# Kernel optimization log

Measured on AMD Instinct MI355X. Metric: run time of the kernel, lower is better.

Reference implementation:

```python
import jax, jax.numpy as jnp
import numpy as np

B, N, M, D = 8, 4096, 256, 1024
H, HD, ROT = 16, 64, 32  # heads, head_dim, rotary dim (partial_rotary_factor=0.5)
GRID_H = GRID_W = 64     # sqrt(N)
BASE = 10000


def rope_tables_2d(h, w, rot_dim, base=BASE, dtype=jnp.float32):
    # 2D rope: half the rotary channels encode height, half encode width.
    n_freq = rot_dim // 4
    inv = 1.0 / (base ** (jnp.arange(n_freq, dtype=jnp.float32) / n_freq))
    fh = jnp.arange(h, dtype=jnp.float32)[:, None] * inv          # [h, nf]
    fw = jnp.arange(w, dtype=jnp.float32)[:, None] * inv          # [w, nf]
    fh_g = jnp.broadcast_to(fh[:, None, :], (h, w, n_freq))
    fw_g = jnp.broadcast_to(fw[None, :, :], (h, w, n_freq))
    freqs = jnp.concatenate([fh_g, fw_g], -1).reshape(h * w, rot_dim // 2)
    emb = jnp.concatenate([freqs, freqs], -1)                     # [h*w, rot_dim]
    return jnp.cos(emb).astype(dtype), jnp.sin(emb).astype(dtype)


def rotate_half(x):
    x1, x2 = jnp.split(x, 2, axis=-1)
    return jnp.concatenate([-x2, x1], axis=-1)


def layernorm(x, w, b, eps=1e-5):
    mu = x.mean(-1, keepdims=True)
    var = ((x - mu) ** 2).mean(-1, keepdims=True)
    return (x - mu) * jax.lax.rsqrt(var + eps) * w + b


def setup_inputs() -> dict:
    key = jax.random.key(0)
    ks = jax.random.split(key, 5)
    inner = H * HD
    return {
        "x": jax.random.normal(ks[0], (B, N, D), jnp.float32),
        "latents": jax.random.normal(ks[1], (B, M, D), jnp.float32),
        "ln_x_w": jnp.ones((D,), jnp.float32),
        "ln_x_b": jnp.zeros((D,), jnp.float32),
        "ln_l_w": jnp.ones((D,), jnp.float32),
        "ln_l_b": jnp.zeros((D,), jnp.float32),
        "Wq": jax.random.normal(ks[2], (D, inner), jnp.float32) * (D ** -0.5),
        "Wkv": jax.random.normal(ks[3], (D, 2 * inner), jnp.float32) * (D ** -0.5),
        "Wo": jax.random.normal(ks[4], (inner, D), jnp.float32) * (inner ** -0.5),
    }


def reference(x, latents, ln_x_w, ln_x_b, ln_l_w, ln_l_b, Wq, Wkv, Wo):
    scale = HD ** -0.5
    xn = layernorm(x, ln_x_w, ln_x_b)
    ln = layernorm(latents, ln_l_w, ln_l_b)

    q = ln @ Wq                                   # [B, M, H*HD]
    kv_x = xn @ Wkv                               # [B, N, 2*H*HD]
    kv_l = ln @ Wkv                               # [B, M, 2*H*HD]
    k_x, v_x = jnp.split(kv_x, 2, axis=-1)
    k_l, v_l = jnp.split(kv_l, 2, axis=-1)

    def to_bhnd(t, L):
        return t.reshape(t.shape[0], L, H, HD).transpose(0, 2, 1, 3)

    q = to_bhnd(q, M)                             # [B, H, M, HD]
    k_x = to_bhnd(k_x, N)                         # [B, H, N, HD]
    v_x = to_bhnd(v_x, N)
    k_l = to_bhnd(k_l, M)
    v_l = to_bhnd(v_l, M)

    # partial 2D RoPE on input keys only (first ROT channels)
    cos, sin = rope_tables_2d(GRID_H, GRID_W, ROT)  # [N, ROT]
    k_rope, k_pass = k_x[..., :ROT], k_x[..., ROT:]
    k_rope = k_rope * cos + rotate_half(k_rope) * sin
    k_x = jnp.concatenate([k_rope, k_pass], axis=-1)

    k = jnp.concatenate([k_x, k_l], axis=2)       # [B, H, N+M, HD]
    v = jnp.concatenate([v_x, v_l], axis=2)

    sim = jnp.einsum('bhid,bhjd->bhij', q * scale, k)   # [B, H, M, N+M]
    attn = jax.nn.softmax(sim, axis=-1)
    out = jnp.einsum('bhij,bhjd->bhid', attn, v)        # [B, H, M, HD]
    out = out.transpose(0, 2, 1, 3).reshape(out.shape[0], M, H * HD)
    return out @ Wo                                      # [B, M, D]
```

## Files before the change

kernel.cpp:

```cpp
#include <hip/hip_runtime.h>
#include <hip/hip_bf16.h>

#define Bb 8
#define Nn 4096
#define Mm 256
#define Dd 1024
#define Hh 16
#define HDd 64
#define Ss 4352
#define INNERd 1024
#define SPLIT 8

typedef __attribute__((ext_vector_type(4))) float f32x4;
typedef __attribute__((ext_vector_type(8))) short short8;
typedef __attribute__((ext_vector_type(4))) int int4v;

__device__ __forceinline__ float bf2f(short u) {
  union { unsigned int i; float f; } c;
  c.i = ((unsigned int)(unsigned short)u) << 16;
  return c.f;
}
__device__ __forceinline__ short f2bf(float f) {
  union { float f; unsigned int i; } c; c.f = f;
  unsigned int x = c.i;
  x += 0x7fff + ((x >> 16) & 1);
  return (short)(x >> 16);
}
__device__ __forceinline__ void gload16(const short* g, short* l) {
  __builtin_amdgcn_global_load_lds(
      (const __attribute__((address_space(1))) void*)g,
      (__attribute__((address_space(3))) void*)l, 16, 0, 0);
}

__global__ __launch_bounds__(256) void prep_kernel(
    const float* __restrict__ x, const float* __restrict__ lat,
    const float* __restrict__ lnxw, const float* __restrict__ lnxb,
    const float* __restrict__ lnlw, const float* __restrict__ lnlb,
    const float* __restrict__ Wq, const float* __restrict__ Wkv,
    const float* __restrict__ Wo,
    short* __restrict__ xn, short* __restrict__ lnr,
    short* __restrict__ Wqkvt, short* __restrict__ Wot) {
  __shared__ float shbuf[32 * 33];
  int b = blockIdx.x, t = threadIdx.x;
  if (b < 34816) {
    const float *src, *w, *bv; short* dst; int row;
    if (b < 32768) { src = x;   w = lnxw; bv = lnxb; dst = xn;  row = b; }
    else           { src = lat; w = lnlw; bv = lnlb; dst = lnr; row = b - 32768; }
    const float4* x4 = (const float4*)(src + (size_t)row * Dd);
    float4 v = x4[t];
    float s  = v.x + v.y + v.z + v.w;
    float ss = v.x*v.x + v.y*v.y + v.z*v.z + v.w*v.w;
#pragma unroll
    for (int o = 1; o < 64; o <<= 1) {
      s  += __shfl_xor(s,  o, 64);
      ss += __shfl_xor(ss, o, 64);
    }
    int wv = t >> 6;
    if ((t & 63) == 0) { shbuf[wv] = s; shbuf[4 + wv] = ss; }
    __syncthreads();
    float tot  = shbuf[0] + shbuf[1] + shbuf[2] + shbuf[3];
    float tot2 = shbuf[4] + shbuf[5] + shbuf[6] + shbuf[7];
    float mean = tot * (1.0f / Dd);
    float var  = tot2 * (1.0f / Dd) - mean * mean;
    float inv  = rsqrtf(var + 1e-5f);
    float4 wv4 = ((const float4*)w)[t];
    float4 bv4 = ((const float4*)bv)[t];
    short4 o4;
    o4.x = f2bf((v.x - mean) * inv * wv4.x + bv4.x);
    o4.y = f2bf((v.y - mean) * inv * wv4.y + bv4.y);
    o4.z = f2bf((v.z - mean) * inv * wv4.z + bv4.z);
    o4.w = f2bf((v.w - mean) * inv * wv4.w + bv4.w);
    *(short4*)(dst + (size_t)row * Dd + t * 4) = o4;
  } else {
    int tb = b - 34816;
    const float* src; short* dst; int Ncol, bx, by;
    if (tb < 1024)      { src = Wq;  dst = Wqkvt; Ncol = 1024; bx = tb & 31; by = tb >> 5; }
    else if (tb < 3072) { int u = tb - 1024; src = Wkv; dst = Wqkvt + (size_t)1024 * 1024; Ncol = 2048; bx = u & 63; by = u >> 6; }
    else                { int u = tb - 3072; src = Wo;  dst = Wot; Ncol = 1024; bx = u & 31; by = u >> 5; }
    int tx = t & 31, ty = t >> 5;
#pragma unroll
    for (int i = 0; i < 32; i += 8)
      shbuf[(ty + i) * 33 + tx] = src[(size_t)(by * 32 + ty + i) * Ncol + bx * 32 + tx];
    __syncthreads();
#pragma unroll
    for (int i = 0; i < 32; i += 8)
      dst[(size_t)(bx * 32 + ty + i) * 1024 + by * 32 + tx] = f2bf(shbuf[tx * 33 + ty + i]);
  }
}

__global__ __launch_bounds__(256, 4) void gemm_fused_kernel(
    const short* __restrict__ xn, const short* __restrict__ lnr,
    const short* __restrict__ Wkvt, const short* __restrict__ Wqkvt,
    short* __restrict__ qdst, short* __restrict__ kdst, short* __restrict__ vdst) {
  __shared__ __align__(16) short Asm[128 * 64];
  __shared__ __align__(16) short Bsm[128 * 64];
  __shared__ float ctab[1024];
  int t = threadIdx.x;
  int wave = t >> 6, lane = t & 63;
  int wm = (wave >> 1) * 64, wn = (wave & 1) * 64;
  int lr = lane & 15, lg = lane >> 4;
  bool big = (int)blockIdx.x < 4096;
  const short* A  = big ? xn  : lnr;
  const short* Bt = big ? Wkvt : Wqkvt;
  int bid = big ? blockIdx.x : blockIdx.x - 4096;
  int nwg = big ? 4096 : 384;
  int ncp = big ? 16 : 24;
  int cpx = nwg >> 3;
  int swz = (bid & 7) * cpx + (bid >> 3);
  int colp = swz % ncp, rowp = swz / ncp;
  int brow = rowp * 128, bcol = colp * 128;
  if (big) {
#pragma unroll
    for (int i = t; i < 512; i += 256) {
      int pos = i >> 3, f = i & 7;
      float ang = (float)pos * exp2f(-1.6609640474436813f * (float)f);
      ctab[i] = cosf(ang);
      ctab[512 + i] = sinf(ang);
    }
  }
  f32x4 acc[4][4] = {};
  for (int kt = 0; kt < 1024; kt += 64) {
    __syncthreads();
#pragma unroll
    for (int u = 0; u < 4; u++) {
      int cid = t + u * 256;
      int r = cid >> 3, c = cid & 7;
      int cl = c ^ (r & 7);
      gload16(A + (size_t)(brow + r) * 1024 + kt + cl * 8, Asm + cid * 8);
      gload16(Bt + (size_t)(bcol + r) * 1024 + kt + cl * 8, Bsm + cid * 8);
    }
    __syncthreads();
#pragma unroll
    for (int ks = 0; ks < 2; ks++) {
      short8 a[4], b[4];
#pragma unroll
      for (int i = 0; i < 4; i++) {
        int ra = wm + i * 16 + lr;
        a[i] = *(const short8*)(Asm + ra * 64 + (((ks * 4 + lg) ^ (ra & 7)) * 8));
        int rb = wn + i * 16 + lr;
        b[i] = *(const short8*)(Bsm + rb * 64 + (((ks * 4 + lg) ^ (rb & 7)) * 8));
      }
#pragma unroll
      for (int mi = 0; mi < 4; mi++)
#pragma unroll
        for (int ni = 0; ni < 4; ni++)
          acc[mi][ni] = __builtin_amdgcn_mfma_f32_16x16x32_bf16(a[mi], b[ni], acc[mi][ni], 0, 0, 0);
    }
  }
  int cbase = bcol + wn;
  if (big) {
    bool kreg = cbase < 1024;
    short* dstp = kreg ? kdst : vdst;
    int h = (cbase & 1023) >> 6;
#pragma unroll
    for (int mi = 0; mi < 4; mi++)
#pragma unroll
      for (int rr = 0; rr < 4; rr++) {
        int row = brow + wm + mi * 16 + lg * 4 + rr;
        int bb = row >> 12, n = row & 4095;
        float v[4];
#pragma unroll
        for (int ni = 0; ni < 4; ni++) v[ni] = acc[mi][ni][rr];
        if (kreg) {
          int pos = (lr & 8) ? (n & 63) : (n >> 6);
          float cs = ctab[pos * 8 + (lr & 7)];
          float sn = ctab[512 + pos * 8 + (lr & 7)];
          float v0 = v[0], v1 = v[1];
          v[0] = v0 * cs - v1 * sn;
          v[1] = v1 * cs + v0 * sn;
        }
        size_t rb = (((size_t)(bb * Hh + h)) * Ss + n) * HDd;
#pragma unroll
        for (int ni = 0; ni < 4; ni++)
          dstp[rb + ni * 16 + lr] = f2bf(v[ni]);
      }
  } else {
#pragma unroll
    for (int mi = 0; mi < 4; mi++)
#pragma unroll
      for (int rr = 0; rr < 4; rr++) {
        int row = brow + wm + mi * 16 + lg * 4 + rr;
        int bb = row >> 8, m = row & 255;
        float v[4];
#pragma unroll
        for (int ni = 0; ni < 4; ni++) v[ni] = acc[mi][ni][rr];
        if (cbase < 1024) {
          int h = cbase >> 6;
          size_t rb = (((size_t)(bb * Hh + h)) * Mm + m) * HDd;
#pragma unroll
          for (int ni = 0; ni < 4; ni++)
            qdst[rb + ni * 16 + lr] = f2bf(v[ni] * 0.18033688f);
        } else if (cbase < 2048) {
          int h = (cbase - 1024) >> 6;
          size_t rb = (((size_t)(bb * Hh + h)) * Ss + (Nn + m)) * HDd;
#pragma unroll
          for (int ni = 0; ni < 4; ni++)
            kdst[rb + ni * 16 + lr] = f2bf(v[ni]);
        } else {
          int h = (cbase - 2048) >> 6;
          size_t rb = (((size_t)(bb * Hh + h)) * Ss + (Nn + m)) * HDd;
#pragma unroll
          for (int ni = 0; ni < 4; ni++)
            vdst[rb + ni * 16 + lr] = f2bf(v[ni]);
        }
      }
  }
}

__global__ __launch_bounds__(256, 4) void gemm_out_kernel(
    const short* __restrict__ A, const short* __restrict__ Bt,
    float* __restrict__ C, int ncp) {
  __shared__ __align__(16) short Asm[128 * 64];
  __shared__ __align__(16) short Bsm[128 * 64];
  int t = threadIdx.x;
  int wave = t >> 6, lane = t & 63;
  int wm = (wave >> 1) * 64, wn = (wave & 1) * 64;
  int lr = lane & 15, lg = lane >> 4;
  int nwg = gridDim.x;
  int cpx = nwg >> 3;
  int swz = (blockIdx.x & 7) * cpx + (blockIdx.x >> 3);
  int colp = swz % ncp, rowp = swz / ncp;
  int brow = rowp * 128, bcol = colp * 128;
  f32x4 acc[4][4] = {};
  for (int kt = 0; kt < 1024; kt += 64) {
    __syncthreads();
#pragma unroll
    for (int u = 0; u < 4; u++) {
      int cid = t + u * 256;
      int r = cid >> 3, c = cid & 7;
      int cl = c ^ (r & 7);
      gload16(A + (size_t)(brow + r) * 1024 + kt + cl * 8, Asm + cid * 8);
      gload16(Bt + (size_t)(bcol + r) * 1024 + kt + cl * 8, Bsm + cid * 8);
    }
    __syncthreads();
#pragma unroll
    for (int ks = 0; ks < 2; ks++) {
      short8 a[4], b[4];
#pragma unroll
      for (int i = 0; i < 4; i++) {
        int ra = wm + i * 16 + lr;
        a[i] = *(const short8*)(Asm + ra * 64 + (((ks * 4 + lg) ^ (ra & 7)) * 8));
        int rb = wn + i * 16 + lr;
        b[i] = *(const short8*)(Bsm + rb * 64 + (((ks * 4 + lg) ^ (rb & 7)) * 8));
      }
#pragma unroll
      for (int mi = 0; mi < 4; mi++)
#pragma unroll
        for (int ni = 0; ni < 4; ni++)
          acc[mi][ni] = __builtin_amdgcn_mfma_f32_16x16x32_bf16(a[mi], b[ni], acc[mi][ni], 0, 0, 0);
    }
  }
#pragma unroll
  for (int mi = 0; mi < 4; mi++)
#pragma unroll
    for (int ni = 0; ni < 4; ni++)
#pragma unroll
      for (int r = 0; r < 4; r++) {
        int row = brow + wm + mi * 16 + lg * 4 + r;
        int col = bcol + wn + ni * 16 + lr;
        C[(size_t)row * 1024 + col] = acc[mi][ni][r];
      }
}

__global__ __launch_bounds__(512) void attn_kernel(const short* __restrict__ qb,
                            const short* __restrict__ kb,
                            const short* __restrict__ vb,
                            short* __restrict__ pO,
                            float* __restrict__ pS) {
  __shared__ __align__(16) short Ksm[64 * 64];
  __shared__ __align__(16) short Vsm[64 * 64];
  int blk = blockIdx.x;
  int sp = blk & (SPLIT - 1), bh = blk >> 3;
  int t = threadIdx.x, wave = t >> 6, lane = t & 63;
  int lr = lane & 15, lg = lane >> 4;
  int q0 = wave * 32;
  const short* qptr = qb + (size_t)bh * Mm * HDd;
  short8 qf[2][2];
#pragma unroll
  for (int qi = 0; qi < 2; qi++)
#pragma unroll
    for (int ks = 0; ks < 2; ks++)
      qf[qi][ks] = *(const short8*)(qptr + (size_t)(q0 + qi * 16 + lr) * HDd + ks * 32 + lg * 8);
  f32x4 accOT[4][2] = {};
  float psq[2] = {0.0f, 0.0f};
  const short* kbase = kb + (size_t)bh * Ss * HDd;
  const short* vbase = vb + (size_t)bh * Ss * HDd;
  int tile0 = (sp * 68) >> 3, tile1 = ((sp + 1) * 68) >> 3;
  for (int tt = tile0; tt < tile1; tt++) {
    int kt = tt * 64;
    __syncthreads();
    {
      int r = t >> 3, c = t & 7;
      int cl = c ^ (r & 7);
      gload16(kbase + (size_t)(kt + r) * HDd + cl * 8, Ksm + t * 8);
      short8 vv = *(const short8*)(vbase + (size_t)(kt + r) * HDd + c * 8);
      int sc = ((r >> 5) << 2) | ((r >> 2) & 3);
      int sw = (((r >> 4) & 1) << 2) | (r & 3);
#pragma unroll
      for (int e = 0; e < 8; e++) {
        int d = c * 8 + e;
        Vsm[d * 64 + ((sc ^ (d & 7)) * 8) + sw] = vv[e];
      }
    }
    __syncthreads();
    f32x4 accST[4][2] = {};
#pragma unroll
    for (int ks = 0; ks < 2; ks++) {
      short8 ka[4];
#pragma unroll
      for (int ji = 0; ji < 4; ji++) {
        int j = ji * 16 + lr;
        int cd = ks * 4 + lg;
        ka[ji] = *(const short8*)(Ksm + j * 64 + ((cd ^ (j & 7)) * 8));
      }
#pragma unroll
      for (int ji = 0; ji < 4; ji++)
#pragma unroll
        for (int qi = 0; qi < 2; qi++)
          accST[ji][qi] = __builtin_amdgcn_mfma_f32_16x16x32_bf16(ka[ji], qf[qi][ks], accST[ji][qi], 0, 0, 0);
    }
    short8 pb[2][2];
#pragma unroll
    for (int qi = 0; qi < 2; qi++) {
#pragma unroll
      for (int ji = 0; ji < 4; ji++)
#pragma unroll
        for (int r = 0; r < 4; r++) {
          float pv = exp2f(accST[ji][qi][r]);
          accST[ji][qi][r] = pv;
          psq[qi] += pv;
        }
#pragma unroll
      for (int s = 0; s < 2; s++)
#pragma unroll
        for (int r = 0; r < 4; r++) {
          pb[s][qi][r]     = f2bf(accST[2 * s][qi][r]);
          pb[s][qi][4 + r] = f2bf(accST[2 * s + 1][qi][r]);
        }
    }
#pragma unroll
    for (int s = 0; s < 2; s++) {
      short8 va[4];
#pragma unroll
      for (int di = 0; di < 4; di++) {
        int d = di * 16 + lr;
        int ck = s * 4 + lg;
        va[di] = *(const short8*)(Vsm + d * 64 + ((ck ^ (d & 7)) * 8));
      }
#pragma unroll
      for (int di = 0; di < 4; di++)
#pragma unroll
        for (int qi = 0; qi < 2; qi++)
          accOT[di][qi] = __builtin_amdgcn_mfma_f32_16x16x32_bf16(va[di], pb[s][qi], accOT[di][qi], 0, 0, 0);
    }
  }
#pragma unroll
  for (int qi = 0; qi < 2; qi++) {
    psq[qi] += __shfl_xor(psq[qi], 16, 64);
    psq[qi] += __shfl_xor(psq[qi], 32, 64);
  }
  size_t base = (size_t)blk * 256;
  if (lane < 16) {
#pragma unroll
    for (int qi = 0; qi < 2; qi++)
      pS[base + q0 + qi * 16 + lr] = psq[qi];
  }
  short* poB = pO + base * 64;
#pragma unroll
  for (int di = 0; di < 4; di++)
#pragma unroll
    for (int qi = 0; qi < 2; qi++)
#pragma unroll
      for (int r = 0; r < 4; r++)
        poB[(size_t)(di * 16 + lg * 4 + r) * 256 + q0 + qi * 16 + lr] = f2bf(accOT[di][qi][r]);
}

__global__ void attn_combine(const short* __restrict__ pO, const float* __restrict__ pS,
                             short* __restrict__ ob) {
  int blk = blockIdx.x;
  int bh = blk >> 1, dh = (blk & 1) << 5;
  int q = threadIdx.x;
  float den = 0.0f;
  float acc[32] = {};
#pragma unroll
  for (int s = 0; s < SPLIT; s++) {
    size_t b2 = (size_t)(bh * SPLIT + s);
    den += pS[b2 * 256 + q];
    const short* po = pO + b2 * 16384 + (size_t)dh * 256;
#pragma unroll
    for (int d = 0; d < 32; d++) acc[d] += bf2f(po[d * 256 + q]);
  }
  float rden = 1.0f / den;
  int b = bh >> 4, h = bh & 15;
  short* dst = ob + ((size_t)(b * Mm + q)) * INNERd + h * HDd + dh;
#pragma unroll
  for (int c = 0; c < 4; c++) {
    short8 o8;
#pragma unroll
    for (int e = 0; e < 8; e++) o8[e] = f2bf(acc[c * 8 + e] * rden);
    *(short8*)(dst + c * 8) = o8;
  }
}

extern "C" void kernel_launch(void* const* d_in, const int* in_sizes, int n_in,
                              void* d_out, int out_size, void* d_ws, size_t ws_size,
                              hipStream_t stream) {
  const float* x    = (const float*)d_in[0];
  const float* lat  = (const float*)d_in[1];
  const float* lnxw = (const float*)d_in[2];
  const float* lnxb = (const float*)d_in[3];
  const float* lnlw = (const float*)d_in[4];
  const float* lnlb = (const float*)d_in[5];
  const float* Wq   = (const float*)d_in[6];
  const float* Wkv  = (const float*)d_in[7];
  const float* Wo   = (const float*)d_in[8];
  char* w = (char*)d_ws;
  const size_t MB = 1048576;
  short* Wqkvt = (short*)(w + 0 * MB);
  short* Wot   = (short*)(w + 6 * MB);
  short* xn    = (short*)(w + 8 * MB);
  short* lnr   = (short*)(w + 72 * MB);
  short* qbuf  = (short*)(w + 76 * MB);
  short* kbuf  = (short*)(w + 80 * MB);
  short* vbuf  = (short*)(w + 148 * MB);
  short* aout  = (short*)(w + 216 * MB);
  short* pO    = (short*)(w + 8 * MB);
  float* pS    = (float*)(w + 72 * MB);

  prep_kernel<<<dim3(38912), dim3(256), 0, stream>>>(
      x, lat, lnxw, lnxb, lnlw, lnlb, Wq, Wkv, Wo, xn, lnr, Wqkvt, Wot);
  gemm_fused_kernel<<<dim3(4480), dim3(256), 0, stream>>>(
      xn, lnr, Wqkvt + (size_t)1024 * 1024, Wqkvt, qbuf, kbuf, vbuf);
  attn_kernel<<<dim3(Bb * Hh * SPLIT), dim3(512), 0, stream>>>(qbuf, kbuf, vbuf, pO, pS);
  attn_combine<<<dim3(256), dim3(256), 0, stream>>>(pO, pS, aout);
  gemm_out_kernel<<<dim3(128), dim3(256), 0, stream>>>(aout, Wot, (float*)d_out, 8);
}
```

Before: 304.5 us.

## Double-buffer K/V shared-memory tiles in attention kernel to overlap loads with MFMA

Attention kernel now keeps two LDS buffers for K and V. It prefetches the next tile, with K via async global-to-LDS and V into registers, while computing on the current tile, and writes the transposed V into the other buffer after the MFMAs. This cuts one barrier per iteration and hides global load latency behind compute. The cost is doubled LDS use (32KB) and extra registers for the prefetched V, which may reduce occupancy.

```diff
diff --git a/kernel.cpp b/kernel.cpp
--- a/kernel.cpp
+++ b/kernel.cpp
@@ -267,8 +267,8 @@
                             const short* __restrict__ vb,
                             short* __restrict__ pO,
                             float* __restrict__ pS) {
-  __shared__ __align__(16) short Ksm[64 * 64];
-  __shared__ __align__(16) short Vsm[64 * 64];
+  __shared__ __align__(16) short Ksm[2][64 * 64];
+  __shared__ __align__(16) short Vsm[2][64 * 64];
   int blk = blockIdx.x;
   int sp = blk & (SPLIT - 1), bh = blk >> 3;
   int t = threadIdx.x, wave = t >> 6, lane = t & 63;
@@ -286,23 +286,31 @@
   const short* kbase = kb + (size_t)bh * Ss * HDd;
   const short* vbase = vb + (size_t)bh * Ss * HDd;
   int tile0 = (sp * 68) >> 3, tile1 = ((sp + 1) * 68) >> 3;
-  for (int tt = tile0; tt < tile1; tt++) {
-    int kt = tt * 64;
-    __syncthreads();
-    {
-      int r = t >> 3, c = t & 7;
-      int cl = c ^ (r & 7);
-      gload16(kbase + (size_t)(kt + r) * HDd + cl * 8, Ksm + t * 8);
-      short8 vv = *(const short8*)(vbase + (size_t)(kt + r) * HDd + c * 8);
-      int sc = ((r >> 5) << 2) | ((r >> 2) & 3);
-      int sw = (((r >> 4) & 1) << 2) | (r & 3);
-#pragma unroll
-      for (int e = 0; e < 8; e++) {
-        int d = c * 8 + e;
-        Vsm[d * 64 + ((sc ^ (d & 7)) * 8) + sw] = vv[e];
-      }
-    }
-    __syncthreads();
+  int sr = t >> 3, scol = t & 7;
+  int scl = scol ^ (sr & 7);
+  int ssc = ((sr >> 5) << 2) | ((sr >> 2) & 3);
+  int ssw = (((sr >> 4) & 1) << 2) | (sr & 3);
+  {
+    int kt = tile0 * 64;
+    gload16(kbase + (size_t)(kt + sr) * HDd + scl * 8, &Ksm[0][t * 8]);
+    short8 vv = *(const short8*)(vbase + (size_t)(kt + sr) * HDd + scol * 8);
+#pragma unroll
+    for (int e = 0; e < 8; e++) {
+      int d = scol * 8 + e;
+      Vsm[0][d * 64 + ((ssc ^ (d & 7)) * 8) + ssw] = vv[e];
+    }
+  }
+  __syncthreads();
+  int cur = 0;
+  for (int tt = tile0; tt < tile1; tt++, cur ^= 1) {
+    int nxt = cur ^ 1;
+    bool pf = (tt + 1 < tile1);
+    short8 vnx;
+    if (pf) {
+      int kn = (tt + 1) * 64;
+      gload16(kbase + (size_t)(kn + sr) * HDd + scl * 8, &Ksm[nxt][t * 8]);
+      vnx = *(const short8*)(vbase + (size_t)(kn + sr) * HDd + scol * 8);
+    }
     f32x4 accST[4][2] = {};
 #pragma unroll
     for (int ks = 0; ks < 2; ks++) {
@@ -311,7 +319,7 @@
       for (int ji = 0; ji < 4; ji++) {
         int j = ji * 16 + lr;
         int cd = ks * 4 + lg;
-        ka[ji] = *(const short8*)(Ksm + j * 64 + ((cd ^ (j & 7)) * 8));
+        ka[ji] = *(const short8*)(&Ksm[cur][0] + j * 64 + ((cd ^ (j & 7)) * 8));
       }
 #pragma unroll
       for (int ji = 0; ji < 4; ji++)
@@ -345,7 +353,7 @@
       for (int di = 0; di < 4; di++) {
         int d = di * 16 + lr;
         int ck = s * 4 + lg;
-        va[di] = *(const short8*)(Vsm + d * 64 + ((ck ^ (d & 7)) * 8));
+        va[di] = *(const short8*)(&Vsm[cur][0] + d * 64 + ((ck ^ (d & 7)) * 8));
       }
 #pragma unroll
       for (int di = 0; di < 4; di++)
@@ -353,6 +361,14 @@
         for (int qi = 0; qi < 2; qi++)
           accOT[di][qi] = __builtin_amdgcn_mfma_f32_16x16x32_bf16(va[di], pb[s][qi], accOT[di][qi], 0, 0, 0);
     }
+    if (pf) {
+#pragma unroll
+      for (int e = 0; e < 8; e++) {
+        int d = scol * 8 + e;
+        Vsm[nxt][d * 64 + ((ssc ^ (d & 7)) * 8) + ssw] = vnx[e];
+      }
+    }
+    __syncthreads();
   }
 #pragma unroll
   for (int qi = 0; qi < 2; qi++) {
```

After: 325.0 us. 1.07x slower.
